# Kernel tuning notes

Measured on AMD Instinct MI355X. Metric: run time of the kernel, lower is better.

The kernel has to match this reference:

```python
import jax, jax.numpy as jnp
import numpy as np

D = 512; H = 2048; NH = 8; NL = 6; VX = 32000; VY = 32000
B = 256; SX = 15; SY = 17; PAD = 0; DH = D // NH


def _pe_table(seq_len, d):
    pos = np.arange(seq_len, dtype=np.float32)[:, None]
    div = 1.0 / (10000.0 ** (np.arange(0, d, 2, dtype=np.float32) / d))
    pe = np.zeros((seq_len, d), dtype=np.float32)
    pe[:, 0::2] = np.sin(pos * div)
    pe[:, 1::2] = np.cos(pos * div)
    return jnp.asarray(pe)


def _ln(x, g, b, eps=1e-5):
    m = x.mean(-1, keepdims=True)
    v = ((x - m) ** 2).mean(-1, keepdims=True)
    return g * (x - m) / jnp.sqrt(v + eps) + b


def _attn(xq, xkv, mask, w, b):
    # w: [4, D, D] (q,k,v,o), b: [4, D]; mask broadcastable to [B,NH,Sq,Sk]
    bs, sq, _ = xq.shape
    sk = xkv.shape[1]
    q = (xq @ w[0] + b[0]).reshape(bs, sq, NH, DH).transpose(0, 2, 1, 3)
    k = (xkv @ w[1] + b[1]).reshape(bs, sk, NH, DH).transpose(0, 2, 1, 3)
    v = (xkv @ w[2] + b[2]).reshape(bs, sk, NH, DH).transpose(0, 2, 1, 3)
    s = jnp.einsum('bhqd,bhkd->bhqk', q, k) / np.sqrt(float(DH))
    s = jnp.where(mask == 0.0, -1e9, s)
    p = jax.nn.softmax(s, axis=-1)
    o = jnp.einsum('bhqk,bhkd->bhqd', p, v).transpose(0, 2, 1, 3).reshape(bs, sq, D)
    return o @ w[3] + b[3]


def setup_inputs():
    key = jax.random.key(0)
    ks = jax.random.split(key, 24)
    s = 0.02
    x = jax.random.randint(ks[0], (B, SX), 0, VX)
    y = jax.random.randint(ks[1], (B, SY), 0, VY)
    emb_x = (jax.random.normal(ks[2], (VX, D)) * s).at[PAD].set(0.0)
    emb_y = (jax.random.normal(ks[3], (VY, D)) * s).at[PAD].set(0.0)
    inp = dict(x=x, y=y, emb_x=emb_x, emb_y=emb_y)
    inp['enc_attn_w'] = jax.random.normal(ks[4], (NL, 4, D, D)) * s
    inp['enc_attn_b'] = jnp.zeros((NL, 4, D))
    inp['enc_ln'] = jnp.stack([jnp.ones((NL, 2, D)), jnp.zeros((NL, 2, D))], axis=2)  # [NL,2,2,D] (g,b)
    inp['enc_ffn_w0'] = jax.random.normal(ks[5], (NL, D, H)) * s
    inp['enc_ffn_b0'] = jnp.zeros((NL, H))
    inp['enc_ffn_w1'] = jax.random.normal(ks[6], (NL, H, D)) * s
    inp['enc_ffn_b1'] = jnp.zeros((NL, D))
    inp['dec_attn_w'] = jax.random.normal(ks[7], (NL, 8, D, D)) * s  # self q,k,v,o then cross q,k,v,o
    inp['dec_attn_b'] = jnp.zeros((NL, 8, D))
    inp['dec_ln'] = jnp.stack([jnp.ones((NL, 3, D)), jnp.zeros((NL, 3, D))], axis=2)  # [NL,3,2,D]
    inp['dec_ffn_w0'] = jax.random.normal(ks[8], (NL, D, H)) * s
    inp['dec_ffn_b0'] = jnp.zeros((NL, H))
    inp['dec_ffn_w1'] = jax.random.normal(ks[9], (NL, H, D)) * s
    inp['dec_ffn_b1'] = jnp.zeros((NL, D))
    inp['fc_w'] = jax.random.normal(ks[10], (D, VY)) * s
    inp['fc_b'] = jnp.zeros((VY,))
    return inp


def reference(x, y, emb_x, emb_y, enc_attn_w, enc_attn_b, enc_ln,
              enc_ffn_w0, enc_ffn_b0, enc_ffn_w1, enc_ffn_b1,
              dec_attn_w, dec_attn_b, dec_ln,
              dec_ffn_w0, dec_ffn_b0, dec_ffn_w1, dec_ffn_b1,
              fc_w, fc_b):
    pe = _pe_table(max(SX, SY + 1), D)
    mask_x = (x != PAD).astype(jnp.float32)[:, None, None, :]        # [B,1,1,SX]
    mask_pad = (y != PAD).astype(jnp.float32)[:, None, None, :]       # [B,1,1,SY]
    mask_y = mask_pad * jnp.tril(jnp.ones((SY, SY), jnp.float32))     # [B,1,SY,SY]

    hx = emb_x[x] + pe[:SX]
    for i in range(NL):
        a = _attn(hx, hx, mask_x, enc_attn_w[i], enc_attn_b[i])
        h0 = _ln(hx + a, enc_ln[i, 0, 0], enc_ln[i, 0, 1])
        f = jax.nn.relu(h0 @ enc_ffn_w0[i] + enc_ffn_b0[i]) @ enc_ffn_w1[i] + enc_ffn_b1[i]
        hx = _ln(h0 + f, enc_ln[i, 1, 0], enc_ln[i, 1, 1])

    hy = emb_y[y] + pe[:SY]
    for i in range(NL):
        a = _attn(hy, hy, mask_y, dec_attn_w[i, :4], dec_attn_b[i, :4])
        h0 = _ln(hy + a, dec_ln[i, 0, 0], dec_ln[i, 0, 1])
        c = _attn(h0, hx, mask_x, dec_attn_w[i, 4:], dec_attn_b[i, 4:])
        h1 = _ln(h0 + c, dec_ln[i, 1, 0], dec_ln[i, 1, 1])
        f = jax.nn.relu(h1 @ dec_ffn_w0[i] + dec_ffn_b0[i]) @ dec_ffn_w1[i] + dec_ffn_b1[i]
        hy = _ln(h1 + f, dec_ln[i, 2, 0], dec_ln[i, 2, 1])

    return hy @ fc_w + fc_b  # [B, SY, VY]
```

## Files before the change

### kernel.cpp

```cpp
#include <hip/hip_runtime.h>
#include <hip/hip_bf16.h>
#include <stdint.h>
#include <type_traits>

typedef __hip_bfloat16 bf16;
typedef __attribute__((ext_vector_type(8))) short bf16x8;
typedef __attribute__((ext_vector_type(4))) float f32x4;

#define DMODEL 512
#define HFF    2048
#define NHEADS 8
#define NLAYERS 6
#define DHEAD  64
#define BATCH  256
#define SXLEN  15
#define SYLEN  17

__device__ __forceinline__ float us2f(unsigned short u) {
  union { unsigned int i; float f; } c; c.i = ((unsigned int)u) << 16; return c.f;
}
__device__ __forceinline__ unsigned short f2us(float f) {
  bf16 h = __float2bfloat16(f);
  return *reinterpret_cast<unsigned short*>(&h);
}
__device__ __forceinline__ float b2f(bf16 v) { return __bfloat162float(v); }

__device__ __forceinline__ void gload_lds16(const void* g, void* l) {
  __builtin_amdgcn_global_load_lds(
      (const __attribute__((address_space(1))) unsigned int*)g,
      (__attribute__((address_space(3))) unsigned int*)l, 16, 0, 0);
}

template<int RELU, int MT, int NT, int WM, int WN, int ZMAP, int BIAS, int XSWZ, typename OT>
__global__ __launch_bounds__(WM * WN * 64) void gemm_t(
    const bf16* __restrict__ A, const bf16* __restrict__ Wt,
    const float* __restrict__ bias, OT* __restrict__ C,
    int M, int N, int K, int ldk,
    long long wStride, long long bStride, long long cStride)
{
  constexpr int BK  = 64;
  constexpr int TH  = WM * WN * 64;
  constexpr int RB  = BK * 2;
  constexpr int MF  = MT / WM / 16;
  constexpr int NF  = NT / WN / 16;
  constexpr int WRS = MT / WM;
  constexpr int WCS = NT / WN;
  constexpr int ABY = MT * RB;
  constexpr int BBY = NT * RB;

  const int z = blockIdx.z;
  long long koff = 0;
  if (ZMAP == 1) {
    int idx = (z >> 1) * 8 + 5 + (z & 1);
    Wt   += (long long)idx * wStride;
    bias += (long long)idx * bStride;
  } else if (ZMAP == 2) {
    koff = (long long)z * K;
  } else {
    Wt   += (long long)z * wStride;
    bias += (long long)z * bStride;
  }
  C += (long long)z * cStride;

  int bid = (int)blockIdx.y * (int)gridDim.x + (int)blockIdx.x;
  if (XSWZ) {
    const int nwg = (int)gridDim.x * (int)gridDim.y;
    const int q = nwg >> 3, r = nwg & 7;
    const int xcd = bid & 7, i = bid >> 3;
    bid = (xcd < r ? xcd * (q + 1) : r * (q + 1) + (xcd - r) * q) + i;
  }
  const int bx = bid % (int)gridDim.x;
  const int by = bid / (int)gridDim.x;

  __shared__ __align__(16) char lds[ABY + BBY];
  const int t    = threadIdx.x;
  const int m0   = by * MT, n0 = bx * NT;
  const int wid  = t >> 6, lane = t & 63;
  const int wm   = wid / WN, wn = wid % WN;
  const int g    = lane >> 4, r = lane & 15;

  f32x4 acc[MF][NF];
  #pragma unroll
  for (int i = 0; i < MF; ++i)
    #pragma unroll
    for (int j = 0; j < NF; ++j) acc[i][j] = (f32x4)0.f;

  const char* Ab = (const char*)(A  + (long long)m0 * ldk + koff);
  const char* Bb = (const char*)(Wt + (long long)n0 * ldk + koff);
  const int rowBytes = ldk * 2;
  const int rdsw = (r & 7) << 4;

  for (int kt = 0; kt < K; kt += BK) {
    __syncthreads();
    #pragma unroll
    for (int off = 0; off < ABY; off += TH * 16) {
      int o = off + t * 16;
      int row = o >> 7, cb = (o & 127) ^ ((row & 7) << 4);
      gload_lds16(Ab + (long long)row * rowBytes + kt * 2 + cb, lds + o);
    }
    #pragma unroll
    for (int off = 0; off < BBY; off += TH * 16) {
      int o = off + t * 16;
      int row = o >> 7, cb = (o & 127) ^ ((row & 7) << 4);
      gload_lds16(Bb + (long long)row * rowBytes + kt * 2 + cb, lds + ABY + o);
    }
    __syncthreads();

    #pragma unroll
    for (int kh = 0; kh < BK / 32; ++kh) {
      bf16x8 af[MF], bfr[NF];
      #pragma unroll
      for (int ms = 0; ms < MF; ++ms)
        af[ms] = *(const bf16x8*)(lds + (wm * WRS + ms * 16 + r) * RB + ((kh * 64 + g * 16) ^ rdsw));
      #pragma unroll
      for (int ns = 0; ns < NF; ++ns)
        bfr[ns] = *(const bf16x8*)(lds + ABY + (wn * WCS + ns * 16 + r) * RB + ((kh * 64 + g * 16) ^ rdsw));
      #pragma unroll
      for (int ms = 0; ms < MF; ++ms)
        #pragma unroll
        for (int ns = 0; ns < NF; ++ns)
          acc[ms][ns] = __builtin_amdgcn_mfma_f32_16x16x32_bf16(af[ms], bfr[ns], acc[ms][ns], 0, 0, 0);
    }
  }

  #pragma unroll
  for (int ms = 0; ms < MF; ++ms) {
    int rowb = m0 + wm * WRS + ms * 16 + g * 4;
    #pragma unroll
    for (int ns = 0; ns < NF; ++ns) {
      int col = n0 + wn * WCS + ns * 16 + r;
      float bv = BIAS ? bias[col] : 0.f;
      f32x4 v = acc[ms][ns];
      #pragma unroll
      for (int j = 0; j < 4; ++j) {
        float o = v[j] + bv;
        if (RELU) o = fmaxf(o, 0.f);
        if constexpr (std::is_same<OT, float>::value)
          C[(long long)(rowb + j) * N + col] = o;
        else
          C[(long long)(rowb + j) * N + col] = __float2bfloat16(o);
      }
    }
  }
}

__global__ __launch_bounds__(256) void transpose_cast2(
    const float* __restrict__ inA, const float* __restrict__ inB, int zSplit,
    bf16* __restrict__ out, int K, int N)
{
  __shared__ unsigned short tile[32][33];
  int z = blockIdx.z;
  const float* ip = (z < zSplit) ? inA + (long long)z * K * N
                                 : inB + (long long)(z - zSplit) * K * N;
  unsigned short* op = (unsigned short*)out + (long long)z * K * N;
  int nx = blockIdx.x * 32, ky = blockIdx.y * 32;
  int tx = threadIdx.x, ty = threadIdx.y;
  #pragma unroll
  for (int j = 0; j < 4; ++j)
    tile[ty + j * 8][tx] = f2us(ip[(long long)(ky + ty + j * 8) * N + nx + tx]);
  __syncthreads();
  #pragma unroll
  for (int j = 0; j < 4; ++j)
    op[(long long)(nx + ty + j * 8) * K + ky + tx] = tile[tx][ty + j * 8];
}

__global__ __launch_bounds__(64) void embed2_k(
    const int* __restrict__ xids, const int* __restrict__ yids,
    const float* __restrict__ ex, const float* __restrict__ ey,
    bf16* __restrict__ ox, bf16* __restrict__ oy)
{
  int row = blockIdx.x;
  const int* ids; const float* emb; bf16* out; int S;
  if (row < BATCH * SXLEN) { ids = xids; emb = ex; out = ox; S = SXLEN; }
  else { row -= BATCH * SXLEN; ids = yids; emb = ey; out = oy; S = SYLEN; }
  int s = row % S;
  int lane = threadIdx.x;
  int id = ids[row];
  const float* e = emb + (long long)id * DMODEL;
  unsigned short* o = (unsigned short*)(out + (long long)row * DMODEL);
  #pragma unroll
  for (int j = 0; j < 8; ++j) {
    int d  = lane * 8 + j;
    int jj = d >> 1;
    float freq = __expf(-(float)(2 * jj) * (9.210340371976184f / 512.f));
    float ang  = (float)s * freq;
    float pe   = (d & 1) ? cosf(ang) : sinf(ang);
    o[d] = f2us(e[d] + pe);
  }
}

template<int CAUSAL>
__global__ __launch_bounds__(64) void attn_core(
    const bf16* __restrict__ Q, const bf16* __restrict__ Kk, const bf16* __restrict__ V,
    const int* __restrict__ tok, bf16* __restrict__ O, int Sq, int Sk)
{
  int bh = blockIdx.x; int b = bh >> 3; int h = bh & 7;
  __shared__ float Qs[SYLEN][DHEAD + 1], Ks[SYLEN][DHEAD + 1], Vs[SYLEN][DHEAD + 1];
  __shared__ float P[SYLEN][SYLEN + 1];
  __shared__ float msk[SYLEN];
  int t = threadIdx.x;

  for (int idx = t; idx < Sq * DHEAD; idx += 64) {
    int q = idx >> 6, d = idx & 63;
    Qs[q][d] = b2f(Q[((long long)(b * Sq + q)) * DMODEL + h * DHEAD + d]);
  }
  for (int idx = t; idx < Sk * DHEAD; idx += 64) {
    int k = idx >> 6, d = idx & 63;
    Ks[k][d] = b2f(Kk[((long long)(b * Sk + k)) * DMODEL + h * DHEAD + d]);
    Vs[k][d] = b2f(V [((long long)(b * Sk + k)) * DMODEL + h * DHEAD + d]);
  }
  if (t < Sk) msk[t] = (tok[b * Sk + t] != 0) ? 1.f : 0.f;
  __syncthreads();

  for (int idx = t; idx < Sq * Sk; idx += 64) {
    int q = idx / Sk, k = idx - q * Sk;
    float s = 0.f;
    #pragma unroll
    for (int i = 0; i < DHEAD; ++i) s += Qs[q][i] * Ks[k][i];
    s *= 0.125f;
    bool m = (msk[k] != 0.f) && (!CAUSAL || k <= q);
    P[q][k] = m ? s : -1e9f;
  }
  __syncthreads();

  if (t < Sq) {
    float mx = -1e30f;
    for (int k = 0; k < Sk; ++k) mx = fmaxf(mx, P[t][k]);
    float sum = 0.f;
    for (int k = 0; k < Sk; ++k) { float e = __expf(P[t][k] - mx); P[t][k] = e; sum += e; }
    float inv = 1.f / sum;
    for (int k = 0; k < Sk; ++k) P[t][k] *= inv;
  }
  __syncthreads();

  int d = t;
  for (int q = 0; q < Sq; ++q) {
    float o = 0.f;
    for (int k = 0; k < Sk; ++k) o += P[q][k] * Vs[k][d];
    O[((long long)(b * Sq + q)) * DMODEL + h * DHEAD + d] = __float2bfloat16(o);
  }
}

__global__ __launch_bounds__(64) void add_ln3_k(
    const bf16* __restrict__ R, const float* __restrict__ P, long long pStride,
    const float* __restrict__ bias,
    const float* __restrict__ gam, const float* __restrict__ bet,
    bf16* __restrict__ out)
{
  long long row = blockIdx.x;
  int lane = threadIdx.x;
  union { uint4 u; unsigned short s[8]; } ua, uo;
  ua.u = ((const uint4*)(R + row * DMODEL))[lane];
  const float4* p0 = (const float4*)(P + row * DMODEL);
  const float4* p1 = (const float4*)(P + pStride + row * DMODEL);
  float4 a0 = p0[lane * 2], a1 = p0[lane * 2 + 1];
  float4 c0 = p1[lane * 2], c1 = p1[lane * 2 + 1];
  float4 bi0 = ((const float4*)bias)[lane * 2], bi1 = ((const float4*)bias)[lane * 2 + 1];
  float pa[8] = {a0.x, a0.y, a0.z, a0.w, a1.x, a1.y, a1.z, a1.w};
  float pc[8] = {c0.x, c0.y, c0.z, c0.w, c1.x, c1.y, c1.z, c1.w};
  float pb[8] = {bi0.x, bi0.y, bi0.z, bi0.w, bi1.x, bi1.y, bi1.z, bi1.w};
  float x[8]; float s = 0.f, sq = 0.f;
  #pragma unroll
  for (int j = 0; j < 8; ++j) {
    x[j] = us2f(ua.s[j]) + pa[j] + pc[j] + pb[j];
    s += x[j]; sq += x[j] * x[j];
  }
  #pragma unroll
  for (int o = 32; o > 0; o >>= 1) { s += __shfl_xor(s, o); sq += __shfl_xor(sq, o); }
  float mean = s * (1.f / DMODEL);
  float var  = sq * (1.f / DMODEL) - mean * mean;
  float inv  = rsqrtf(var + 1e-5f);
  float4 g0 = ((const float4*)gam)[lane * 2], g1 = ((const float4*)gam)[lane * 2 + 1];
  float4 b0 = ((const float4*)bet)[lane * 2], b1 = ((const float4*)bet)[lane * 2 + 1];
  float gg[8] = {g0.x, g0.y, g0.z, g0.w, g1.x, g1.y, g1.z, g1.w};
  float bb[8] = {b0.x, b0.y, b0.z, b0.w, b1.x, b1.y, b1.z, b1.w};
  #pragma unroll
  for (int j = 0; j < 8; ++j)
    uo.s[j] = f2us(gg[j] * (x[j] - mean) * inv + bb[j]);
  ((uint4*)(out + row * DMODEL))[lane] = uo.u;
}

extern "C" void kernel_launch(void* const* d_in, const int* in_sizes, int n_in,
                              void* d_out, int out_size, void* d_ws, size_t ws_size,
                              hipStream_t stream)
{
  const int*   x        = (const int*)  d_in[0];
  const int*   y        = (const int*)  d_in[1];
  const float* emb_x    = (const float*)d_in[2];
  const float* emb_y    = (const float*)d_in[3];
  const float* enc_attn_w = (const float*)d_in[4];
  const float* enc_attn_b = (const float*)d_in[5];
  const float* enc_ln     = (const float*)d_in[6];
  const float* enc_f0w    = (const float*)d_in[7];
  const float* enc_f0b    = (const float*)d_in[8];
  const float* enc_f1w    = (const float*)d_in[9];
  const float* enc_f1b    = (const float*)d_in[10];
  const float* dec_attn_w = (const float*)d_in[11];
  const float* dec_attn_b = (const float*)d_in[12];
  const float* dec_ln     = (const float*)d_in[13];
  const float* dec_f0w    = (const float*)d_in[14];
  const float* dec_f0b    = (const float*)d_in[15];
  const float* dec_f1w    = (const float*)d_in[16];
  const float* dec_f1b    = (const float*)d_in[17];
  const float* fc_w       = (const float*)d_in[18];
  const float* fc_b       = (const float*)d_in[19];

  const int MX = BATCH * SXLEN;
  const int MY = BATCH * SYLEN;
  const long long DD = (long long)DMODEL * DMODEL;
  const long long SMEL = (long long)MY * DMODEL;
  const long long MXEL = (long long)MX * DMODEL;
  const long long FFEL = (long long)DMODEL * HFF;
  const long long PST  = (long long)MY * DMODEL;

  char* p = (char*)d_ws;
  auto alloc = [&](long long elems) -> bf16* {
    bf16* r = (bf16*)p; p += ((elems * 2 + 255) / 256) * 256; return r;
  };
  bf16* wt_attn = alloc(72 * DD);
  bf16* wt_f0   = alloc(12 * FFEL);
  bf16* wt_f1   = alloc(12 * FFEL);
  bf16* wt_fc   = alloc(32000LL * DMODEL);
  bf16* hx  = alloc(SMEL);
  bf16* hy  = alloc(SMEL);
  bf16* qb  = alloc(3 * SMEL);
  bf16* ao  = alloc(SMEL);
  bf16* h0  = alloc(SMEL);
  bf16* h1  = alloc(SMEL);
  bf16* mid = alloc((long long)MY * HFF);
  bf16* ckv = alloc(12 * MXEL);
  float* fp = (float*)alloc(2LL * MY * DMODEL * 2);
  if ((size_t)(p - (char*)d_ws) > ws_size) return;

  bf16* wt_enc_attn = wt_attn;
  bf16* wt_dec_attn = wt_attn + 24 * DD;
  bf16* wt_enc_f0   = wt_f0;
  bf16* wt_dec_f0   = wt_f0 + 6 * FFEL;
  bf16* wt_enc_f1   = wt_f1;
  bf16* wt_dec_f1   = wt_f1 + 6 * FFEL;

  dim3 tb(32, 8);
  transpose_cast2<<<dim3(16, 16, 72), tb, 0, stream>>>(enc_attn_w, dec_attn_w, 24, wt_attn, DMODEL, DMODEL);
  transpose_cast2<<<dim3(64, 16, 12), tb, 0, stream>>>(enc_f0w, dec_f0w, 6, wt_f0, DMODEL, HFF);
  transpose_cast2<<<dim3(16, 64, 12), tb, 0, stream>>>(enc_f1w, dec_f1w, 6, wt_f1, HFF, DMODEL);
  transpose_cast2<<<dim3(1000, 16, 1), tb, 0, stream>>>(fc_w, fc_w, 1, wt_fc, DMODEL, 32000);

  embed2_k<<<MX + MY, 64, 0, stream>>>(x, y, emb_x, emb_y, hx, hy);

  for (int i = 0; i < NLAYERS; ++i) {
    const bf16*  Wl = wt_enc_attn + (long long)i * 4 * DD;
    const float* Bl = enc_attn_b + (long long)i * 4 * DMODEL;
    const float* Lg = enc_ln + (size_t)i * 2048;
    gemm_t<0, 64, 64, 2, 2, 0, 1, 1, bf16><<<dim3(8, 60, 3), 256, 0, stream>>>(hx, Wl, Bl, qb,
        MX, DMODEL, DMODEL, DMODEL, DD, DMODEL, SMEL);
    attn_core<0><<<BATCH * NHEADS, 64, 0, stream>>>(qb, qb + SMEL, qb + 2 * SMEL, x, ao, SXLEN, SXLEN);
    gemm_t<0, 64, 64, 2, 2, 2, 0, 1, float><<<dim3(8, 60, 2), 256, 0, stream>>>(ao,
        Wl + 3 * DD, Bl + 3 * DMODEL, fp, MX, DMODEL, 256, DMODEL, 0, 0, PST);
    add_ln3_k<<<MX, 64, 0, stream>>>(hx, fp, PST, Bl + 3 * DMODEL, Lg, Lg + 512, h0);
    gemm_t<1, 128, 128, 2, 2, 0, 1, 1, bf16><<<dim3(16, 30, 1), 256, 0, stream>>>(h0,
        wt_enc_f0 + (long long)i * FFEL, enc_f0b + (long long)i * HFF, mid,
        MX, HFF, DMODEL, DMODEL, 0, 0, 0);
    gemm_t<0, 64, 64, 2, 2, 2, 0, 1, float><<<dim3(8, 60, 2), 256, 0, stream>>>(mid,
        wt_enc_f1 + (long long)i * FFEL, enc_f1b, fp,
        MX, DMODEL, 1024, HFF, 0, 0, PST);
    add_ln3_k<<<MX, 64, 0, stream>>>(h0, fp, PST,
        enc_f1b + (long long)i * DMODEL, Lg + 1024, Lg + 1536, hx);
  }

  gemm_t<0, 64, 64, 2, 2, 1, 1, 1, bf16><<<dim3(8, 60, 12), 256, 0, stream>>>(hx, wt_dec_attn,
      dec_attn_b, ckv, MX, DMODEL, DMODEL, DMODEL, DD, DMODEL, MXEL);

  for (int i = 0; i < NLAYERS; ++i) {
    const bf16*  Wl = wt_dec_attn + (long long)i * 8 * DD;
    const float* Bl = dec_attn_b + (long long)i * 8 * DMODEL;
    const float* Lg = dec_ln + (size_t)i * 3072;
    gemm_t<0, 64, 64, 2, 2, 0, 1, 1, bf16><<<dim3(8, 68, 3), 256, 0, stream>>>(hy, Wl, Bl, qb,
        MY, DMODEL, DMODEL, DMODEL, DD, DMODEL, SMEL);
    attn_core<1><<<BATCH * NHEADS, 64, 0, stream>>>(qb, qb + SMEL, qb + 2 * SMEL, y, ao, SYLEN, SYLEN);
    gemm_t<0, 64, 64, 2, 2, 2, 0, 1, float><<<dim3(8, 68, 2), 256, 0, stream>>>(ao,
        Wl + 3 * DD, Bl + 3 * DMODEL, fp, MY, DMODEL, 256, DMODEL, 0, 0, PST);
    add_ln3_k<<<MY, 64, 0, stream>>>(hy, fp, PST, Bl + 3 * DMODEL, Lg, Lg + 512, h0);
    gemm_t<0, 64, 64, 2, 2, 0, 1, 1, bf16><<<dim3(8, 68, 1), 256, 0, stream>>>(h0, Wl + 4 * DD, Bl + 4 * DMODEL, qb,
        MY, DMODEL, DMODEL, DMODEL, 0, 0, 0);
    attn_core<0><<<BATCH * NHEADS, 64, 0, stream>>>(qb, ckv + (long long)(2 * i) * MXEL,
        ckv + (long long)(2 * i + 1) * MXEL, x, ao, SYLEN, SXLEN);
    gemm_t<0, 64, 64, 2, 2, 2, 0, 1, float><<<dim3(8, 68, 2), 256, 0, stream>>>(ao,
        Wl + 7 * DD, Bl + 7 * DMODEL, fp, MY, DMODEL, 256, DMODEL, 0, 0, PST);
    add_ln3_k<<<MY, 64, 0, stream>>>(h0, fp, PST, Bl + 7 * DMODEL, Lg + 1024, Lg + 1536, h0);
    gemm_t<1, 128, 128, 2, 2, 0, 1, 1, bf16><<<dim3(16, 34, 1), 256, 0, stream>>>(h0,
        wt_dec_f0 + (long long)i * FFEL, dec_f0b + (long long)i * HFF, mid,
        MY, HFF, DMODEL, DMODEL, 0, 0, 0);
    gemm_t<0, 64, 64, 2, 2, 2, 0, 1, float><<<dim3(8, 68, 2), 256, 0, stream>>>(mid,
        wt_dec_f1 + (long long)i * FFEL, dec_f1b, fp,
        MY, DMODEL, 1024, HFF, 0, 0, PST);
    add_ln3_k<<<MY, 64, 0, stream>>>(h0, fp, PST,
        dec_f1b + (long long)i * DMODEL, Lg + 2048, Lg + 2560, hy);
  }

  gemm_t<0, 256, 256, 4, 2, 0, 1, 1, float><<<dim3(125, 17, 1), 512, 0, stream>>>(hy, wt_fc, fc_b,
      (float*)d_out, MY, 32000, DMODEL, DMODEL, 0, 0, 0);
}
```

Before: 1.795 ms.

## Fuse split-K GEMM with residual-add LayerNorm via last-block atomic counter

Replaces the split-K output-projection and FFN-down GEMMs followed by a separate add+LayerNorm kernel with one fused kernel. Each block writes its partial tile, then bumps a per-row-tile atomic counter, and the last of the 16 blocks (8 column tiles times 2 K halves) for that row tile performs the residual+bias+LayerNorm for its 64 rows. This drops 24 kernel launches and their inter-kernel gaps. In exchange it adds threadfences, an atomic per block, a serial LN tail run by one block per row tile, and a counter buffer that must be reset and shared across launches.

```diff
diff --git a/kernel.cpp b/kernel.cpp
--- a/kernel.cpp
+++ b/kernel.cpp
@@ -49,13 +49,10 @@
   constexpr int BBY = NT * RB;
 
   const int z = blockIdx.z;
-  long long koff = 0;
   if (ZMAP == 1) {
     int idx = (z >> 1) * 8 + 5 + (z & 1);
     Wt   += (long long)idx * wStride;
     bias += (long long)idx * bStride;
-  } else if (ZMAP == 2) {
-    koff = (long long)z * K;
   } else {
     Wt   += (long long)z * wStride;
     bias += (long long)z * bStride;
@@ -85,8 +82,8 @@
     #pragma unroll
     for (int j = 0; j < NF; ++j) acc[i][j] = (f32x4)0.f;
 
-  const char* Ab = (const char*)(A  + (long long)m0 * ldk + koff);
-  const char* Bb = (const char*)(Wt + (long long)n0 * ldk + koff);
+  const char* Ab = (const char*)(A  + (long long)m0 * ldk);
+  const char* Bb = (const char*)(Wt + (long long)n0 * ldk);
   const int rowBytes = ldk * 2;
   const int rdsw = (r & 7) << 4;
 
@@ -142,6 +139,131 @@
       }
     }
   }
+}
+
+__global__ __launch_bounds__(256) void gemm_skln(
+    const bf16* __restrict__ A, const bf16* __restrict__ Wt,
+    float* __restrict__ P, int M, int Khalf, int ldk, long long pStride,
+    const bf16* __restrict__ R, const float* __restrict__ biasLN,
+    const float* __restrict__ gam, const float* __restrict__ bet,
+    bf16* __restrict__ out, int* __restrict__ cnt)
+{
+  constexpr int RB = 128, ABY = 64 * RB, BBY = 64 * RB;
+  const int z = blockIdx.z;
+  const long long koff = (long long)z * Khalf;
+  float* C = P + (long long)z * pStride;
+
+  int bid = (int)blockIdx.y * (int)gridDim.x + (int)blockIdx.x;
+  { const int nwg = (int)gridDim.x * (int)gridDim.y;
+    const int q = nwg >> 3, r2 = nwg & 7;
+    const int xcd = bid & 7, i = bid >> 3;
+    bid = (xcd < r2 ? xcd * (q + 1) : r2 * (q + 1) + (xcd - r2) * q) + i; }
+  const int bx = bid % (int)gridDim.x;
+  const int by = bid / (int)gridDim.x;
+
+  __shared__ __align__(16) char lds[ABY + BBY];
+  const int t = threadIdx.x, wid = t >> 6, lane = t & 63;
+  const int wm = wid >> 1, wn = wid & 1, g = lane >> 4, r = lane & 15;
+
+  f32x4 acc[2][2];
+  #pragma unroll
+  for (int i = 0; i < 2; ++i)
+    #pragma unroll
+    for (int j = 0; j < 2; ++j) acc[i][j] = (f32x4)0.f;
+
+  const int m0 = by * 64, n0 = bx * 64;
+  const char* Ab = (const char*)(A  + (long long)m0 * ldk + koff);
+  const char* Bb = (const char*)(Wt + (long long)n0 * ldk + koff);
+  const int rowBytes = ldk * 2;
+  const int rdsw = (r & 7) << 4;
+
+  for (int kt = 0; kt < Khalf; kt += 64) {
+    __syncthreads();
+    #pragma unroll
+    for (int off = 0; off < ABY; off += 256 * 16) {
+      int o = off + t * 16;
+      int row = o >> 7, cb = (o & 127) ^ ((row & 7) << 4);
+      gload_lds16(Ab + (long long)row * rowBytes + kt * 2 + cb, lds + o);
+    }
+    #pragma unroll
+    for (int off = 0; off < BBY; off += 256 * 16) {
+      int o = off + t * 16;
+      int row = o >> 7, cb = (o & 127) ^ ((row & 7) << 4);
+      gload_lds16(Bb + (long long)row * rowBytes + kt * 2 + cb, lds + ABY + o);
+    }
+    __syncthreads();
+
+    #pragma unroll
+    for (int kh = 0; kh < 2; ++kh) {
+      bf16x8 af[2], bfr[2];
+      #pragma unroll
+      for (int ms = 0; ms < 2; ++ms)
+        af[ms] = *(const bf16x8*)(lds + (wm * 32 + ms * 16 + r) * RB + ((kh * 64 + g * 16) ^ rdsw));
+      #pragma unroll
+      for (int ns = 0; ns < 2; ++ns)
+        bfr[ns] = *(const bf16x8*)(lds + ABY + (wn * 32 + ns * 16 + r) * RB + ((kh * 64 + g * 16) ^ rdsw));
+      #pragma unroll
+      for (int ms = 0; ms < 2; ++ms)
+        #pragma unroll
+        for (int ns = 0; ns < 2; ++ns)
+          acc[ms][ns] = __builtin_amdgcn_mfma_f32_16x16x32_bf16(af[ms], bfr[ns], acc[ms][ns], 0, 0, 0);
+    }
+  }
+
+  #pragma unroll
+  for (int ms = 0; ms < 2; ++ms) {
+    int rowb = m0 + wm * 32 + ms * 16 + g * 4;
+    #pragma unroll
+    for (int ns = 0; ns < 2; ++ns) {
+      int col = n0 + wn * 32 + ns * 16 + r;
+      f32x4 v = acc[ms][ns];
+      #pragma unroll
+      for (int j = 0; j < 4; ++j)
+        C[(long long)(rowb + j) * 512 + col] = v[j];
+    }
+  }
+
+  __threadfence();
+  __shared__ int isLast;
+  if (t == 0) isLast = (atomicAdd(&cnt[by], 1) == 15) ? 1 : 0;
+  __syncthreads();
+  if (!isLast) return;
+  __threadfence();
+
+  for (int rr = wid; rr < 64; rr += 4) {
+    long long row = m0 + rr;
+    union { uint4 u; unsigned short s[8]; } ua, uo;
+    ua.u = ((const uint4*)(R + row * DMODEL))[lane];
+    const float4* p0 = (const float4*)(P + row * DMODEL);
+    const float4* p1 = (const float4*)(P + pStride + row * DMODEL);
+    float4 a0 = p0[lane * 2], a1 = p0[lane * 2 + 1];
+    float4 c0 = p1[lane * 2], c1 = p1[lane * 2 + 1];
+    float4 bi0 = ((const float4*)biasLN)[lane * 2], bi1 = ((const float4*)biasLN)[lane * 2 + 1];
+    float pa[8] = {a0.x, a0.y, a0.z, a0.w, a1.x, a1.y, a1.z, a1.w};
+    float pc[8] = {c0.x, c0.y, c0.z, c0.w, c1.x, c1.y, c1.z, c1.w};
+    float pb[8] = {bi0.x, bi0.y, bi0.z, bi0.w, bi1.x, bi1.y, bi1.z, bi1.w};
+    float xv[8]; float s = 0.f, sq = 0.f;
+    #pragma unroll
+    for (int j = 0; j < 8; ++j) {
+      xv[j] = us2f(ua.s[j]) + pa[j] + pc[j] + pb[j];
+      s += xv[j]; sq += xv[j] * xv[j];
+    }
+    #pragma unroll
+    for (int o = 32; o > 0; o >>= 1) { s += __shfl_xor(s, o); sq += __shfl_xor(sq, o); }
+    float mean = s * (1.f / DMODEL);
+    float var  = sq * (1.f / DMODEL) - mean * mean;
+    float inv  = rsqrtf(var + 1e-5f);
+    float4 g0 = ((const float4*)gam)[lane * 2], g1 = ((const float4*)gam)[lane * 2 + 1];
+    float4 b0 = ((const float4*)bet)[lane * 2], b1 = ((const float4*)bet)[lane * 2 + 1];
+    float gg[8] = {g0.x, g0.y, g0.z, g0.w, g1.x, g1.y, g1.z, g1.w};
+    float bb[8] = {b0.x, b0.y, b0.z, b0.w, b1.x, b1.y, b1.z, b1.w};
+    #pragma unroll
+    for (int j = 0; j < 8; ++j)
+      uo.s[j] = f2us(gg[j] * (xv[j] - mean) * inv + bb[j]);
+    ((uint4*)(out + row * DMODEL))[lane] = uo.u;
+  }
+  __syncthreads();
+  if (t == 0) cnt[by] = 0;
 }
 
 __global__ __launch_bounds__(256) void transpose_cast2(
@@ -239,45 +361,6 @@
     for (int k = 0; k < Sk; ++k) o += P[q][k] * Vs[k][d];
     O[((long long)(b * Sq + q)) * DMODEL + h * DHEAD + d] = __float2bfloat16(o);
   }
-}
-
-__global__ __launch_bounds__(64) void add_ln3_k(
-    const bf16* __restrict__ R, const float* __restrict__ P, long long pStride,
-    const float* __restrict__ bias,
-    const float* __restrict__ gam, const float* __restrict__ bet,
-    bf16* __restrict__ out)
-{
-  long long row = blockIdx.x;
-  int lane = threadIdx.x;
-  union { uint4 u; unsigned short s[8]; } ua, uo;
-  ua.u = ((const uint4*)(R + row * DMODEL))[lane];
-  const float4* p0 = (const float4*)(P + row * DMODEL);
-  const float4* p1 = (const float4*)(P + pStride + row * DMODEL);
-  float4 a0 = p0[lane * 2], a1 = p0[lane * 2 + 1];
-  float4 c0 = p1[lane * 2], c1 = p1[lane * 2 + 1];
-  float4 bi0 = ((const float4*)bias)[lane * 2], bi1 = ((const float4*)bias)[lane * 2 + 1];
-  float pa[8] = {a0.x, a0.y, a0.z, a0.w, a1.x, a1.y, a1.z, a1.w};
-  float pc[8] = {c0.x, c0.y, c0.z, c0.w, c1.x, c1.y, c1.z, c1.w};
-  float pb[8] = {bi0.x, bi0.y, bi0.z, bi0.w, bi1.x, bi1.y, bi1.z, bi1.w};
-  float x[8]; float s = 0.f, sq = 0.f;
-  #pragma unroll
-  for (int j = 0; j < 8; ++j) {
-    x[j] = us2f(ua.s[j]) + pa[j] + pc[j] + pb[j];
-    s += x[j]; sq += x[j] * x[j];
-  }
-  #pragma unroll
-  for (int o = 32; o > 0; o >>= 1) { s += __shfl_xor(s, o); sq += __shfl_xor(sq, o); }
-  float mean = s * (1.f / DMODEL);
-  float var  = sq * (1.f / DMODEL) - mean * mean;
-  float inv  = rsqrtf(var + 1e-5f);
-  float4 g0 = ((const float4*)gam)[lane * 2], g1 = ((const float4*)gam)[lane * 2 + 1];
-  float4 b0 = ((const float4*)bet)[lane * 2], b1 = ((const float4*)bet)[lane * 2 + 1];
-  float gg[8] = {g0.x, g0.y, g0.z, g0.w, g1.x, g1.y, g1.z, g1.w};
-  float bb[8] = {b0.x, b0.y, b0.z, b0.w, b1.x, b1.y, b1.z, b1.w};
-  #pragma unroll
-  for (int j = 0; j < 8; ++j)
-    uo.s[j] = f2us(gg[j] * (x[j] - mean) * inv + bb[j]);
-  ((uint4*)(out + row * DMODEL))[lane] = uo.u;
 }
 
 extern "C" void kernel_launch(void* const* d_in, const int* in_sizes, int n_in,
@@ -330,6 +413,7 @@
   bf16* mid = alloc((long long)MY * HFF);
   bf16* ckv = alloc(12 * MXEL);
   float* fp = (float*)alloc(2LL * MY * DMODEL * 2);
+  int*  cnt = (int*)alloc(256);
   if ((size_t)(p - (char*)d_ws) > ws_size) return;
 
   bf16* wt_enc_attn = wt_attn;
@@ -338,6 +422,8 @@
   bf16* wt_dec_f0   = wt_f0 + 6 * FFEL;
   bf16* wt_enc_f1   = wt_f1;
   bf16* wt_dec_f1   = wt_f1 + 6 * FFEL;
+
+  hipMemsetAsync((void*)cnt, 0, 128 * sizeof(int), stream);
 
   dim3 tb(32, 8);
   transpose_cast2<<<dim3(16, 16, 72), tb, 0, stream>>>(enc_attn_w, dec_attn_w, 24, wt_attn, DMODEL, DMODEL);
@@ -354,17 +440,13 @@
     gemm_t<0, 64, 64, 2, 2, 0, 1, 1, bf16><<<dim3(8, 60, 3), 256, 0, stream>>>(hx, Wl, Bl, qb,
         MX, DMODEL, DMODEL, DMODEL, DD, DMODEL, SMEL);
     attn_core<0><<<BATCH * NHEADS, 64, 0, stream>>>(qb, qb + SMEL, qb + 2 * SMEL, x, ao, SXLEN, SXLEN);
-    gemm_t<0, 64, 64, 2, 2, 2, 0, 1, float><<<dim3(8, 60, 2), 256, 0, stream>>>(ao,
-        Wl + 3 * DD, Bl + 3 * DMODEL, fp, MX, DMODEL, 256, DMODEL, 0, 0, PST);
-    add_ln3_k<<<MX, 64, 0, stream>>>(hx, fp, PST, Bl + 3 * DMODEL, Lg, Lg + 512, h0);
+    gemm_skln<<<dim3(8, 60, 2), 256, 0, stream>>>(ao, Wl + 3 * DD, fp, MX, 256, DMODEL, PST,
+        hx, Bl + 3 * DMODEL, Lg, Lg + 512, h0, cnt);
     gemm_t<1, 128, 128, 2, 2, 0, 1, 1, bf16><<<dim3(16, 30, 1), 256, 0, stream>>>(h0,
         wt_enc_f0 + (long long)i * FFEL, enc_f0b + (long long)i * HFF, mid,
         MX, HFF, DMODEL, DMODEL, 0, 0, 0);
-    gemm_t<0, 64, 64, 2, 2, 2, 0, 1, float><<<dim3(8, 60, 2), 256, 0, stream>>>(mid,
-        wt_enc_f1 + (long long)i * FFEL, enc_f1b, fp,
-        MX, DMODEL, 1024, HFF, 0, 0, PST);
-    add_ln3_k<<<MX, 64, 0, stream>>>(h0, fp, PST,
-        enc_f1b + (long long)i * DMODEL, Lg + 1024, Lg + 1536, hx);
+    gemm_skln<<<dim3(8, 60, 2), 256, 0, stream>>>(mid, wt_enc_f1 + (long long)i * FFEL, fp,
+        MX, 1024, HFF, PST, h0, enc_f1b + (long long)i * DMODEL, Lg + 1024, Lg + 1536, hx, cnt);
   }
 
   gemm_t<0, 64, 64, 2, 2, 1, 1, 1, bf16><<<dim3(8, 60, 12), 256, 0, stream>>>(hx, wt_dec_attn,
@@ -377,24 +459,19 @@
     gemm_t<0, 64, 64, 2, 2, 0, 1, 1, bf16><<<dim3(8, 68, 3), 256, 0, stream>>>(hy, Wl, Bl, qb,
         MY, DMODEL, DMODEL, DMODEL, DD, DMODEL, SMEL);
     attn_core<1><<<BATCH * NHEADS, 64, 0, stream>>>(qb, qb + SMEL, qb + 2 * SMEL, y, ao, SYLEN, SYLEN);
-    gemm_t<0, 64, 64, 2, 2, 2, 0, 1, float><<<dim3(8, 68, 2), 256, 0, stream>>>(ao,
-        Wl + 3 * DD, Bl + 3 * DMODEL, fp, MY, DMODEL, 256, DMODEL, 0, 0, PST);
-    add_ln3_k<<<MY, 64, 0, stream>>>(hy, fp, PST, Bl + 3 * DMODEL, Lg, Lg + 512, h0);
+    gemm_skln<<<dim3(8, 68, 2), 256, 0, stream>>>(ao, Wl + 3 * DD, fp, MY, 256, DMODEL, PST,
+        hy, Bl + 3 * DMODEL, Lg, Lg + 512, h0, cnt);
     gemm_t<0, 64, 64, 2, 2, 0, 1, 1, bf16><<<dim3(8, 68, 1), 256, 0, stream>>>(h0, Wl + 4 * DD, Bl + 4 * DMODEL, qb,
         MY, DMODEL, DMODEL, DMODEL, 0, 0, 0);
     attn_core<0><<<BATCH * NHEADS, 64, 0, stream>>>(qb, ckv + (long long)(2 * i) * MXEL,
         ckv + (long long)(2 * i + 1) * MXEL, x, ao, SYLEN, SXLEN);
-    gemm_t<0, 64, 64, 2, 2, 2, 0, 1, float><<<dim3(8, 68, 2), 256, 0, stream>>>(ao,
-        Wl + 7 * DD, Bl + 7 * DMODEL, fp, MY, DMODEL, 256, DMODEL, 0, 0, PST);
-    add_ln3_k<<<MY, 64, 0, stream>>>(h0, fp, PST, Bl + 7 * DMODEL, Lg + 1024, Lg + 1536, h0);
+    gemm_skln<<<dim3(8, 68, 2), 256, 0, stream>>>(ao, Wl + 7 * DD, fp, MY, 256, DMODEL, PST,
+        h0, Bl + 7 * DMODEL, Lg + 1024, Lg + 1536, h0, cnt);
     gemm_t<1, 128, 128, 2, 2, 0, 1, 1, bf16><<<dim3(16, 34, 1), 256, 0, stream>>>(h0,
         wt_dec_f0 + (long long)i * FFEL, dec_f0b + (long long)i * HFF, mid,
         MY, HFF, DMODEL, DMODEL, 0, 0, 0);
-    gemm_t<0, 64, 64, 2, 2, 2, 0, 1, float><<<dim3(8, 68, 2), 256, 0, stream>>>(mid,
-        wt_dec_f1 + (long long)i * FFEL, dec_f1b, fp,
-        MY, DMODEL, 1024, HFF, 0, 0, PST);
-    add_ln3_k<<<MY, 64, 0, stream>>>(h0, fp, PST,
-        dec_f1b + (long long)i * DMODEL, Lg + 2048, Lg + 2560, hy);
+    gemm_skln<<<dim3(8, 68, 2), 256, 0, stream>>>(mid, wt_dec_f1 + (long long)i * FFEL, fp,
+        MY, 1024, HFF, PST, h0, dec_f1b + (long long)i * DMODEL, Lg + 2048, Lg + 2560, hy, cnt);
   }
 
   gemm_t<0, 256, 256, 4, 2, 0, 1, 1, float><<<dim3(125, 17, 1), 512, 0, stream>>>(hy, wt_fc, fc_b,
```

New measurement: 5.874 ms. 227% more time.
